# Optimization experiments

Hardware: AMD Instinct MI355X
Metric: run time of the kernel (lower is better)

Reference implementation:

```python
import jax, jax.numpy as jnp
import numpy as np

L, V, D = 8, 512, 256            # num_loci, per-locus vocab, embedding_dim
B, K = 8192, 16                  # batch, candidates per sample
HID = 2 * D                      # pooling MLP hidden width


def setup_inputs() -> dict:
    key = jax.random.key(0)
    k_tok, k_tab, k_w1, k_w2 = jax.random.split(key, 4)
    haplotypes = jax.random.randint(k_tok, (B, K, L), 0, V, dtype=jnp.int64)
    # nn.Embedding default init: N(0, 1); padding_idx row zeroed.
    tables = jax.random.normal(k_tab, (L, V, D), dtype=jnp.float32)
    tables = tables.at[:, 0, :].set(0.0)
    # Xavier-uniform for the two Linear layers (stored as [in, out]).
    lim1 = float(np.sqrt(6.0 / (L * D + HID)))
    W1 = jax.random.uniform(k_w1, (L * D, HID), jnp.float32, -lim1, lim1)
    b1 = jnp.zeros((HID,), jnp.float32)
    lim2 = float(np.sqrt(6.0 / (HID + D)))
    W2 = jax.random.uniform(k_w2, (HID, D), jnp.float32, -lim2, lim2)
    b2 = jnp.zeros((D,), jnp.float32)
    return {"haplotypes": haplotypes, "tables": tables,
            "W1": W1, "b1": b1, "W2": W2, "b2": b2}


def reference(haplotypes, tables, W1, b1, W2, b2):
    b, k, num_loci = haplotypes.shape
    vocab = tables.shape[1]
    tok = jnp.clip(haplotypes.reshape(-1, num_loci), 0, vocab - 1)  # [N, L]
    # Per-locus gather, vectorized over loci: [N, L, D]
    emb = tables[jnp.arange(num_loci), tok]
    # padding_idx row is all-zeros; masking keeps forward identical and
    # matches torch's zero-gradient behavior for the padding row.
    emb = emb * (tok != 0)[..., None].astype(emb.dtype)
    x = emb.reshape(emb.shape[0], num_loci * tables.shape[2])  # concat -> [N, L*D]
    h = jax.nn.gelu(x @ W1 + b1, approximate=False)            # torch GELU = erf
    out = h @ W2 + b2                                          # [N, D]
    return out.reshape(b, k, tables.shape[2])
```

## Files before the change

kernel.cpp:

```cpp
#include <hip/hip_runtime.h>
#include <math.h>

typedef __attribute__((ext_vector_type(8))) short  short8;
typedef __attribute__((ext_vector_type(4))) float  floatx4;
typedef __attribute__((ext_vector_type(2))) float  float2v;
typedef __attribute__((ext_vector_type(4))) unsigned int uintx4;

#define NLOCI 8
#define VOCAB 512
#define DDIM  256
#define HID   512
#define NSAMP (8192 * 16)

__device__ __forceinline__ float bitsf(unsigned int u) {
    union { unsigned int u; float f; } c; c.u = u; return c.f;
}
__device__ __forceinline__ unsigned short f2bf(float f) {
    union { float f; unsigned int u; } c; c.f = f;
    unsigned int u = c.u;
    return (unsigned short)((u + 0x7FFFu + ((u >> 16) & 1u)) >> 16);
}
__device__ __forceinline__ unsigned short f2bf_fast(float f) {
    union { float f; unsigned int u; } c; c.f = f;
    return (unsigned short)((c.u + 0x8000u) >> 16);
}
__device__ __forceinline__ float gelu_fast(float x) {
    float t = x * x;
    float y = x * __builtin_fmaf(0.035677408f, t, 0.79788456f);
    float e = __builtin_amdgcn_exp2f(y * 2.8853901f);
    float r = __builtin_amdgcn_rcpf(e + 1.0f);
    return x - x * r;
}
__device__ __forceinline__ void async_copy16(const void* g, void* l) {
    __builtin_amdgcn_global_load_lds(
        (const __attribute__((address_space(1))) unsigned int*)g,
        (__attribute__((address_space(3))) unsigned int*)l, 16, 0, 0);
}

__global__ __launch_bounds__(256) void k_fuse_tables(
    const float* __restrict__ tables,
    const float* __restrict__ W1,
    const float* __restrict__ b1,
    unsigned short* __restrict__ Tp)
{
    const int l  = blockIdx.x >> 6;
    const int v0 = ((blockIdx.x >> 3) & 7) * 64;
    const int n0 = (blockIdx.x & 7) * 64;

    __shared__ unsigned short a_lds[64 * 256];
    __shared__ unsigned short bt_lds[64 * 256];

    const int t = threadIdx.x;

    {
        const float* asrc = tables + (l * 512 + v0) * 256;
#pragma unroll
        for (int i = 0; i < 16; ++i) {
            int flat = i * 1024 + t * 4;
            int row = flat >> 8, k = flat & 255;
            float4 v = *(const float4*)(asrc + flat);
            ushort4 pk4;
            pk4.x = f2bf(v.x); pk4.y = f2bf(v.y); pk4.z = f2bf(v.z); pk4.w = f2bf(v.w);
            int chunkX = (k >> 3) ^ (row & 31);
            *(ushort4*)(a_lds + row * 256 + chunkX * 8 + (k & 7)) = pk4;
        }
    }
    {
        const int n = t & 63;
        const int kq = (t >> 6) * 64;
        const float* bsrc = W1 + (l * 256) * 512 + n0 + n;
#pragma unroll
        for (int i = 0; i < 8; ++i) {
            int k0 = kq + i * 8;
            short8 pk8;
#pragma unroll
            for (int j = 0; j < 8; ++j)
                pk8[j] = (short)f2bf(bsrc[(k0 + j) * 512]);
            int chunkX = (k0 >> 3) ^ (n & 31);
            *(short8*)(bt_lds + n * 256 + chunkX * 8) = pk8;
        }
    }
    __syncthreads();

    const int wave = t >> 6, lane = t & 63;
    const int p = lane & 15, q = lane >> 4;
    const int arow = wave * 16 + p;

    floatx4 acc[4];
#pragma unroll
    for (int nt = 0; nt < 4; ++nt) acc[nt] = (floatx4){0.f, 0.f, 0.f, 0.f};

#pragma unroll
    for (int kc = 0; kc < 8; ++kc) {
        int cq = kc * 4 + q;
        short8 afrag = *(const short8*)(a_lds + arow * 256 + (cq ^ (arow & 31)) * 8);
#pragma unroll
        for (int nt = 0; nt < 4; ++nt) {
            int brow = nt * 16 + p;
            short8 bfrag = *(const short8*)(bt_lds + brow * 256 + (cq ^ (brow & 31)) * 8);
            acc[nt] = __builtin_amdgcn_mfma_f32_16x16x32_bf16(afrag, bfrag, acc[nt], 0, 0, 0);
        }
    }

#pragma unroll
    for (int nt = 0; nt < 4; ++nt) {
        int col = n0 + nt * 16 + p;
        float badd = (l == 0) ? b1[col] : 0.0f;
#pragma unroll
        for (int r = 0; r < 4; ++r) {
            int row = v0 + wave * 16 + q * 4 + r;
            Tp[(l * 512 + row) * 512 + col] = f2bf(acc[nt][r] + badd);
        }
    }
}

__global__ __launch_bounds__(256) void k_transpose_cvt(
    const float* __restrict__ in, unsigned short* __restrict__ out, int R, int C)
{
    __shared__ float tile[64 * 65];
    const int t = threadIdx.x;
    const int r0 = blockIdx.x * 64, c0 = blockIdx.y * 64;

#pragma unroll
    for (int i = 0; i < 16; ++i) {
        int flat = i * 256 + t;
        int rr = flat >> 6, cc = flat & 63;
        tile[rr * 65 + cc] = in[(r0 + rr) * C + c0 + cc];
    }
    __syncthreads();
#pragma unroll
    for (int i = 0; i < 8; ++i) {
        int flat = i * 256 + t;
        int cc = flat >> 5, rp = (flat & 31) * 2;
        ushort2 v;
        v.x = f2bf(tile[rp * 65 + cc]);
        v.y = f2bf(tile[(rp + 1) * 65 + cc]);
        *(ushort2*)(out + (c0 + cc) * R + r0 + rp) = v;
    }
}

__global__ __launch_bounds__(256, 3) void k_main(
    const int* __restrict__ hap,
    const unsigned short* __restrict__ Tp,
    const unsigned short* __restrict__ W2t,
    const float* __restrict__ b2,
    float* __restrict__ out)
{
    __shared__ unsigned short w2_lds[256 * 64];

    const int t = threadIdx.x;
    const int wave = t >> 6, lane = t & 63;
    const int p = lane & 15, q = lane >> 4;
    const int m_base = blockIdx.x * 64 + wave * 16;

    unsigned int goff[8];
    {
        const uintx4* hp = (const uintx4*)(hap + (m_base + p) * 8);
        uintx4 h0 = hp[0], h1 = hp[1];
#pragma unroll
        for (int l = 0; l < 4; ++l) {
            goff[l]     = (unsigned)(l)     * 524288u + (h0[l] & 511u) * 1024u + (unsigned)(q * 16);
            goff[l + 4] = (unsigned)(l + 4) * 524288u + (h1[l] & 511u) * 1024u + (unsigned)(q * 16);
        }
    }
    const char* Tpc = (const char*)Tp;

    const int drow = lane >> 3;
    const int j_sw = (lane & 7) ^ (drow & 7);
    const unsigned short* wsrc = W2t + (wave * 64 + drow) * 512 + j_sw * 8;
    const int p7 = p & 7;

    floatx4 acc[16];
#pragma unroll
    for (int nt = 0; nt < 16; ++nt) acc[nt] = (floatx4){0.f, 0.f, 0.f, 0.f};

    uintx4 ga[8], gb[8];
#pragma unroll
    for (int l = 0; l < 8; ++l)
        ga[l] = *(const uintx4*)(Tpc + goff[l]);

#pragma unroll
    for (int s = 0; s < 16; ++s) {
        if ((s & 1) == 0) {
            const int kb = s >> 1;
            asm volatile("s_waitcnt lgkmcnt(0)" ::: "memory");
            __builtin_amdgcn_s_barrier();
            asm volatile("" ::: "memory");
#pragma unroll
            for (int i = 0; i < 8; ++i)
                async_copy16(wsrc + kb * 64 + i * 8 * 512,
                             w2_lds + (wave * 64 + i * 8) * 64);
            asm volatile("" ::: "memory");
        }

        if (s < 15) {
            const unsigned int koff = (unsigned)(s + 1) * 64u;
#pragma unroll
            for (int l = 0; l < 8; ++l)
                gb[l] = *(const uintx4*)(Tpc + goff[l] + koff);
        }

        short8 afrag;
#pragma unroll
        for (int j = 0; j < 4; ++j) {
            float2v u0 = (float2v){bitsf(ga[0][j] << 16), bitsf(ga[0][j] & 0xFFFF0000u)};
            float2v u1 = (float2v){bitsf(ga[1][j] << 16), bitsf(ga[1][j] & 0xFFFF0000u)};
            float2v u2 = (float2v){bitsf(ga[2][j] << 16), bitsf(ga[2][j] & 0xFFFF0000u)};
            float2v u3 = (float2v){bitsf(ga[3][j] << 16), bitsf(ga[3][j] & 0xFFFF0000u)};
            float2v u4 = (float2v){bitsf(ga[4][j] << 16), bitsf(ga[4][j] & 0xFFFF0000u)};
            float2v u5 = (float2v){bitsf(ga[5][j] << 16), bitsf(ga[5][j] & 0xFFFF0000u)};
            float2v u6 = (float2v){bitsf(ga[6][j] << 16), bitsf(ga[6][j] & 0xFFFF0000u)};
            float2v u7 = (float2v){bitsf(ga[7][j] << 16), bitsf(ga[7][j] & 0xFFFF0000u)};
            float2v sj = ((u0 + u1) + (u2 + u3)) + ((u4 + u5) + (u6 + u7));
            afrag[2 * j]     = (short)f2bf_fast(gelu_fast(sj[0]));
            afrag[2 * j + 1] = (short)f2bf_fast(gelu_fast(sj[1]));
        }

        if (s < 15) {
#pragma unroll
            for (int l = 0; l < 8; ++l) ga[l] = gb[l];
        }

        if ((s & 1) == 0) {
            asm volatile("s_waitcnt vmcnt(8)" ::: "memory");
            __builtin_amdgcn_s_barrier();
            asm volatile("" ::: "memory");
        }

        const unsigned short* bbase =
            w2_lds + p * 64 + ((((s & 1) * 4 + q) ^ p7) * 8);
        __builtin_amdgcn_s_setprio(1);
#pragma unroll
        for (int nt = 0; nt < 16; ++nt) {
            short8 bfrag = *(const short8*)(bbase + nt * 1024);
            acc[nt] = __builtin_amdgcn_mfma_f32_16x16x32_bf16(afrag, bfrag, acc[nt], 0, 0, 0);
        }
        __builtin_amdgcn_s_setprio(0);
    }

#pragma unroll
    for (int nt = 0; nt < 16; ++nt) {
        int n = nt * 16 + p;
        float b2v = b2[n];
#pragma unroll
        for (int r = 0; r < 4; ++r) {
            int m = m_base + q * 4 + r;
            __builtin_nontemporal_store(acc[nt][r] + b2v, out + m * 256 + n);
        }
    }
}

extern "C" void kernel_launch(void* const* d_in, const int* in_sizes, int n_in,
                              void* d_out, int out_size, void* d_ws, size_t ws_size,
                              hipStream_t stream) {
    const int*   hap    = (const int*)d_in[0];
    const float* tables = (const float*)d_in[1];
    const float* W1     = (const float*)d_in[2];
    const float* b1     = (const float*)d_in[3];
    const float* W2     = (const float*)d_in[4];
    const float* b2     = (const float*)d_in[5];
    float*       outp   = (float*)d_out;

    unsigned short* Tp  = (unsigned short*)d_ws;
    unsigned short* W2t = (unsigned short*)d_ws + NLOCI * VOCAB * HID;

    k_fuse_tables<<<dim3(512), dim3(256), 0, stream>>>(tables, W1, b1, Tp);
    k_transpose_cvt<<<dim3(8, 4), dim3(256), 0, stream>>>(W2, W2t, HID, DDIM);
    k_main<<<dim3(NSAMP / 64), dim3(256), 0, stream>>>(hap, Tp, W2t, b2, outp);
}
```

Before: 285.5 us.

## Merge table-fusion and W2 transpose into one prep kernel, add sched barriers

Folds the W2 transpose/convert into the table-fusion kernel as 32 extra blocks, which removes one launch and lets both prep tasks run concurrently. In the main kernel, per-locus gather offsets become precomputed 64-bit pointers, and empty asm memory fences become sched_barrier(0) calls that pin the order of the gather loads and async copies. The new fences may limit compiler interleaving, and the pointers use more registers at an occupancy of 3 waves per SIMD.

```diff
diff --git a/kernel.cpp b/kernel.cpp
--- a/kernel.cpp
+++ b/kernel.cpp
@@ -37,20 +37,46 @@
         (__attribute__((address_space(3))) unsigned int*)l, 16, 0, 0);
 }
 
-__global__ __launch_bounds__(256) void k_fuse_tables(
+__global__ __launch_bounds__(256) void k_prep(
     const float* __restrict__ tables,
     const float* __restrict__ W1,
     const float* __restrict__ b1,
-    unsigned short* __restrict__ Tp)
+    const float* __restrict__ W2,
+    unsigned short* __restrict__ Tp,
+    unsigned short* __restrict__ W2t)
 {
+    __shared__ unsigned short a_lds[64 * 256];
+    __shared__ unsigned short bt_lds[64 * 256];
+
+    const int t = threadIdx.x;
+
+    if (blockIdx.x >= 512) {
+        const int bid = blockIdx.x - 512;
+        const int r0 = (bid & 7) * 64;
+        const int c0 = (bid >> 3) * 64;
+        float* tile = (float*)a_lds;
+#pragma unroll
+        for (int i = 0; i < 16; ++i) {
+            int flat = i * 256 + t;
+            int rr = flat >> 6, cc = flat & 63;
+            tile[rr * 65 + cc] = W2[(r0 + rr) * DDIM + c0 + cc];
+        }
+        __syncthreads();
+#pragma unroll
+        for (int i = 0; i < 8; ++i) {
+            int flat = i * 256 + t;
+            int cc = flat >> 5, rp = (flat & 31) * 2;
+            ushort2 v;
+            v.x = f2bf(tile[rp * 65 + cc]);
+            v.y = f2bf(tile[(rp + 1) * 65 + cc]);
+            *(ushort2*)(W2t + (c0 + cc) * HID + r0 + rp) = v;
+        }
+        return;
+    }
+
     const int l  = blockIdx.x >> 6;
     const int v0 = ((blockIdx.x >> 3) & 7) * 64;
     const int n0 = (blockIdx.x & 7) * 64;
-
-    __shared__ unsigned short a_lds[64 * 256];
-    __shared__ unsigned short bt_lds[64 * 256];
-
-    const int t = threadIdx.x;
 
     {
         const float* asrc = tables + (l * 512 + v0) * 256;
@@ -114,31 +140,6 @@
     }
 }
 
-__global__ __launch_bounds__(256) void k_transpose_cvt(
-    const float* __restrict__ in, unsigned short* __restrict__ out, int R, int C)
-{
-    __shared__ float tile[64 * 65];
-    const int t = threadIdx.x;
-    const int r0 = blockIdx.x * 64, c0 = blockIdx.y * 64;
-
-#pragma unroll
-    for (int i = 0; i < 16; ++i) {
-        int flat = i * 256 + t;
-        int rr = flat >> 6, cc = flat & 63;
-        tile[rr * 65 + cc] = in[(r0 + rr) * C + c0 + cc];
-    }
-    __syncthreads();
-#pragma unroll
-    for (int i = 0; i < 8; ++i) {
-        int flat = i * 256 + t;
-        int cc = flat >> 5, rp = (flat & 31) * 2;
-        ushort2 v;
-        v.x = f2bf(tile[rp * 65 + cc]);
-        v.y = f2bf(tile[(rp + 1) * 65 + cc]);
-        *(ushort2*)(out + (c0 + cc) * R + r0 + rp) = v;
-    }
-}
-
 __global__ __launch_bounds__(256, 3) void k_main(
     const int* __restrict__ hap,
     const unsigned short* __restrict__ Tp,
@@ -153,17 +154,18 @@
     const int p = lane & 15, q = lane >> 4;
     const int m_base = blockIdx.x * 64 + wave * 16;
 
-    unsigned int goff[8];
+    const char* gbase[8];
     {
         const uintx4* hp = (const uintx4*)(hap + (m_base + p) * 8);
         uintx4 h0 = hp[0], h1 = hp[1];
 #pragma unroll
         for (int l = 0; l < 4; ++l) {
-            goff[l]     = (unsigned)(l)     * 524288u + (h0[l] & 511u) * 1024u + (unsigned)(q * 16);
-            goff[l + 4] = (unsigned)(l + 4) * 524288u + (h1[l] & 511u) * 1024u + (unsigned)(q * 16);
-        }
-    }
-    const char* Tpc = (const char*)Tp;
+            gbase[l]     = (const char*)Tp + (unsigned)l       * 524288u
+                         + (h0[l] & 511u) * 1024u + (unsigned)(q * 16);
+            gbase[l + 4] = (const char*)Tp + (unsigned)(l + 4) * 524288u
+                         + (h1[l] & 511u) * 1024u + (unsigned)(q * 16);
+        }
+    }
 
     const int drow = lane >> 3;
     const int j_sw = (lane & 7) ^ (drow & 7);
@@ -177,7 +179,8 @@
     uintx4 ga[8], gb[8];
 #pragma unroll
     for (int l = 0; l < 8; ++l)
-        ga[l] = *(const uintx4*)(Tpc + goff[l]);
+        ga[l] = *(const uintx4*)(gbase[l]);
+    __builtin_amdgcn_sched_barrier(0);
 
 #pragma unroll
     for (int s = 0; s < 16; ++s) {
@@ -185,19 +188,19 @@
             const int kb = s >> 1;
             asm volatile("s_waitcnt lgkmcnt(0)" ::: "memory");
             __builtin_amdgcn_s_barrier();
-            asm volatile("" ::: "memory");
+            __builtin_amdgcn_sched_barrier(0);
 #pragma unroll
             for (int i = 0; i < 8; ++i)
                 async_copy16(wsrc + kb * 64 + i * 8 * 512,
                              w2_lds + (wave * 64 + i * 8) * 64);
-            asm volatile("" ::: "memory");
+            __builtin_amdgcn_sched_barrier(0);
         }
 
         if (s < 15) {
-            const unsigned int koff = (unsigned)(s + 1) * 64u;
 #pragma unroll
             for (int l = 0; l < 8; ++l)
-                gb[l] = *(const uintx4*)(Tpc + goff[l] + koff);
+                gb[l] = *(const uintx4*)(gbase[l] + (s + 1) * 64);
+            __builtin_amdgcn_sched_barrier(0);
         }
 
         short8 afrag;
@@ -224,7 +227,7 @@
         if ((s & 1) == 0) {
             asm volatile("s_waitcnt vmcnt(8)" ::: "memory");
             __builtin_amdgcn_s_barrier();
-            asm volatile("" ::: "memory");
+            __builtin_amdgcn_sched_barrier(0);
         }
 
         const unsigned short* bbase =
@@ -264,7 +267,6 @@
     unsigned short* Tp  = (unsigned short*)d_ws;
     unsigned short* W2t = (unsigned short*)d_ws + NLOCI * VOCAB * HID;
 
-    k_fuse_tables<<<dim3(512), dim3(256), 0, stream>>>(tables, W1, b1, Tp);
-    k_transpose_cvt<<<dim3(8, 4), dim3(256), 0, stream>>>(W2, W2t, HID, DDIM);
+    k_prep<<<dim3(544), dim3(256), 0, stream>>>(tables, W1, b1, W2, Tp, W2t);
     k_main<<<dim3(NSAMP / 64), dim3(256), 0, stream>>>(hap, Tp, W2t, b2, outp);
 }
```

Result: no change. 286.5 us (+0.3%).
